# Kernel tuning notes

Hardware: AMD Instinct MI355X
Metric: run time of the kernel (lower is better)

Reference implementation:

```python
import jax, jax.numpy as jnp
import numpy as np

B, F, S, H1, H2 = 4096, 512, 32, 64, 32


def setup_inputs() -> dict:
    key = jax.random.key(0)
    ks = jax.random.split(key, 9)
    x = jax.random.normal(ks[0], (B, F), dtype=jnp.float32)
    # ExU layer init: truncated_normal(mean=4, std=0.5) on weight, std=0.5 on bias
    W0 = 4.0 + 0.5 * jax.random.normal(ks[1], (F, S, S), dtype=jnp.float32)
    b0 = 0.5 * jax.random.normal(ks[2], (F, S), dtype=jnp.float32)
    # ReLU hidden layers: xavier-ish weights, small biases
    W1 = jax.random.normal(ks[3], (F, S, H1), dtype=jnp.float32) * np.sqrt(2.0 / (S + H1))
    b1 = 0.5 * jax.random.normal(ks[4], (F, S), dtype=jnp.float32)
    W2 = jax.random.normal(ks[5], (F, H1, H2), dtype=jnp.float32) * np.sqrt(2.0 / (H1 + H2))
    b2 = 0.5 * jax.random.normal(ks[6], (F, H1), dtype=jnp.float32)
    Wl = jax.random.normal(ks[7], (F, H2), dtype=jnp.float32) * np.sqrt(2.0 / (H2 + 1))
    out_bias = jnp.zeros((1,), dtype=jnp.float32)
    return {"x": x, "W0": W0, "b0": b0, "W1": W1, "b1": b1,
            "W2": W2, "b2": b2, "Wl": Wl, "out_bias": out_bias}


def reference(x, W0, b0, W1, b1, W2, b2, Wl, out_bias):
    # ExU shallow layer per feature: clip((x_f - b0_f) @ exp(W0_f), 0, 1)
    # x[:, :, None] - b0 broadcasts scalar feature to (B, F, S)
    h = jnp.clip(jnp.einsum('bfs,fsh->bfh', x[:, :, None] - b0[None], jnp.exp(W0)), 0.0, 1.0)
    # ReLU hidden layers: relu((h - b) @ W)
    h = jax.nn.relu(jnp.einsum('bfs,fsh->bfh', h - b1[None], W1))   # (B, F, H1)
    h = jax.nn.relu(jnp.einsum('bfh,fho->bfo', h - b2[None], W2))   # (B, F, H2)
    # per-feature Linear(H2 -> 1, no bias), concatenated over features
    f_out = jnp.einsum('bfo,fo->bf', h, Wl)                          # (B, F)
    # forward_type == 'sum' (feature_dropout is identity at inference)
    return f_out.sum(axis=-1) + out_bias[0], f_out
```

## Files before the change

### kernel.cpp

```cpp
#include <hip/hip_runtime.h>

typedef __attribute__((ext_vector_type(8))) short short8;
typedef __attribute__((ext_vector_type(4))) float f32x4;
typedef unsigned int uint32;

namespace {
constexpr int F = 512, NB = 4096;
constexpr int RB = 256;
constexpr int FPB = 4;
constexpr int NFQ = F / FPB;
constexpr size_t OFF_W1F  = 0;
constexpr size_t OFF_W2F  = OFF_W1F + (size_t)F * 4 * 64 * 16;
constexpr size_t OFF_TAB  = OFF_W2F + (size_t)F * 4 * 64 * 16;
constexpr size_t OFF_PART = OFF_TAB + (size_t)F * 160 * 4;
constexpr size_t WS_NEED  = OFF_PART + (size_t)NFQ * NB * 4;
}

__device__ __forceinline__ uint32 cvtpk(float lo, float hi) {
    uint32 r;
    asm("v_cvt_pk_bf16_f32 %0, %1, %2" : "=v"(r) : "v"(lo), "v"(hi));
    return r;
}
__device__ __forceinline__ float clip01(float v) {
    return __builtin_amdgcn_fmed3f(v, 0.f, 1.f);
}

__global__ __launch_bounds__(256) void nam_prep(
    const float* __restrict__ W0, const float* __restrict__ b0,
    const float* __restrict__ W1, const float* __restrict__ b1,
    const float* __restrict__ W2, const float* __restrict__ b2,
    char* __restrict__ ws)
{
    const int f = blockIdx.x;
    const int t = threadIdx.x;
    const int lane = t & 63, w = t >> 6, g = lane >> 4, rr = lane & 15;

    __shared__ float LW[2048];
    __shared__ float red[256], red2[256];

    const float* W0f = W0 + (size_t)f * 1024;
    const float* W1f = W1 + (size_t)f * 2048;
    const float* W2f = W2 + (size_t)f * 2048;
    float* tab = (float*)(ws + OFF_TAB) + (size_t)f * 160;
    union U8 { uint32 u[4]; short8 s8; };

    *(float4*)&LW[t * 4] = *(const float4*)&W0f[t * 4];
    __syncthreads();
    {
        int j = t & 31, sc = t >> 5;
        float a = 0.f, c = 0.f;
#pragma unroll
        for (int k = 0; k < 4; ++k) {
            int s = sc * 4 + k;
            float e = expf(LW[s * 32 + j]);
            a += e; c += b0[f * 32 + s] * e;
        }
        red[sc * 32 + j] = a; red2[sc * 32 + j] = c;
    }
    __syncthreads();
    if (t < 32) {
        float a = 0.f, c = 0.f;
#pragma unroll
        for (int k = 0; k < 8; ++k) { a += red[k * 32 + t]; c += red2[k * 32 + t]; }
        tab[t] = a; tab[32 + t] = -c;
    }
    __syncthreads();

    *(float4*)&LW[t * 4]        = *(const float4*)&W1f[t * 4];
    *(float4*)&LW[1024 + t * 4] = *(const float4*)&W1f[1024 + t * 4];
    __syncthreads();
    {
        int j = t & 63, sc = t >> 6;
        float d = 0.f;
#pragma unroll
        for (int k = 0; k < 8; ++k) {
            int s = sc * 8 + k;
            d += b1[f * 32 + s] * LW[s * 64 + j];
        }
        red[sc * 64 + j] = d;
    }
    {
        int mi = w;
        int col = 32 * (mi & 1) + 8 * (rr >> 2) + 4 * (mi >> 1) + (rr & 3);
        int base = (8 * g) * 64 + col;
        U8 v;
        v.u[0] = cvtpk(LW[base],       LW[base + 64]);
        v.u[1] = cvtpk(LW[base + 128], LW[base + 192]);
        v.u[2] = cvtpk(LW[base + 256], LW[base + 320]);
        v.u[3] = cvtpk(LW[base + 384], LW[base + 448]);
        ((short8*)(ws + OFF_W1F))[((size_t)f * 4 + mi) * 64 + lane] = v.s8;
    }
    __syncthreads();
    if (t < 64) {
        float d = red[t] + red[64 + t] + red[128 + t] + red[192 + t];
        int dst = 32 * ((t >> 2) & 1) + 16 * (t >> 5) + 4 * ((t >> 3) & 3) + (t & 3);
        tab[64 + dst] = -d;
    }
    __syncthreads();

    *(float4*)&LW[t * 4]        = *(const float4*)&W2f[t * 4];
    *(float4*)&LW[1024 + t * 4] = *(const float4*)&W2f[1024 + t * 4];
    __syncthreads();
    {
        int o = t & 31, hc = t >> 5;
        float d = 0.f;
#pragma unroll
        for (int k = 0; k < 8; ++k) {
            int h = hc * 8 + k;
            d += b2[f * 64 + h] * LW[h * 32 + o];
        }
        red[hc * 32 + o] = d;
    }
    {
        int m2 = w >> 1, kc = w & 1;
        int base = (32 * kc + 8 * g) * 32 + 16 * m2 + rr;
        U8 v;
        v.u[0] = cvtpk(LW[base],       LW[base + 32]);
        v.u[1] = cvtpk(LW[base + 64],  LW[base + 96]);
        v.u[2] = cvtpk(LW[base + 128], LW[base + 160]);
        v.u[3] = cvtpk(LW[base + 192], LW[base + 224]);
        ((short8*)(ws + OFF_W2F))[((size_t)f * 4 + m2 * 2 + kc) * 64 + lane] = v.s8;
    }
    __syncthreads();
    if (t < 32) {
        float d = 0.f;
#pragma unroll
        for (int k = 0; k < 8; ++k) d += red[k * 32 + t];
        tab[128 + t] = -d;
    }
}

__device__ __forceinline__ short8 make_hb(float xv, const f32x4& A0, const f32x4& A1,
                                          const f32x4& C0, const f32x4& C1) {
    union { uint32 u[4]; short8 s8; } hb;
    hb.u[0] = cvtpk(clip01(fmaf(xv, A0[0], C0[0])), clip01(fmaf(xv, A0[1], C0[1])));
    hb.u[1] = cvtpk(clip01(fmaf(xv, A0[2], C0[2])), clip01(fmaf(xv, A0[3], C0[3])));
    hb.u[2] = cvtpk(clip01(fmaf(xv, A1[0], C1[0])), clip01(fmaf(xv, A1[1], C1[1])));
    hb.u[3] = cvtpk(clip01(fmaf(xv, A1[2], C1[2])), clip01(fmaf(xv, A1[3], C1[3])));
    return hb.s8;
}
__device__ __forceinline__ short8 packrelu(const f32x4& x, const f32x4& y) {
    union { uint32 u[4]; short8 s8; } r;
    r.u[0] = cvtpk(fmaxf(x[0], 0.f), fmaxf(x[1], 0.f));
    r.u[1] = cvtpk(fmaxf(x[2], 0.f), fmaxf(x[3], 0.f));
    r.u[2] = cvtpk(fmaxf(y[0], 0.f), fmaxf(y[1], 0.f));
    r.u[3] = cvtpk(fmaxf(y[2], 0.f), fmaxf(y[3], 0.f));
    return r.s8;
}

__global__ __launch_bounds__(256, 4) void nam_main(
    const float* __restrict__ x, const float* __restrict__ Wl,
    const char* __restrict__ ws, float* __restrict__ fout, float* __restrict__ part)
{
    const int fq = blockIdx.y;
    const int f0 = fq * FPB;
    const int rbase = blockIdx.x * RB;
    const int t = threadIdx.x;
    const int w = t >> 6, lane = t & 63;
    const int g = lane >> 4, rr = lane & 15;
    const int f = f0 + w;

    __shared__ float sx[FPB * RB];
    __shared__ float psum[FPB * RB * 4];

    {
        float4 v = *(const float4*)(x + (size_t)(rbase + t) * F + f0);
        sx[0 * RB + t] = v.x; sx[1 * RB + t] = v.y;
        sx[2 * RB + t] = v.z; sx[3 * RB + t] = v.w;
    }

    const short8* w1img = (const short8*)(ws + OFF_W1F);
    const short8* w2img = (const short8*)(ws + OFF_W2F);
    short8 w1f[4], w2f[2][2];
#pragma unroll
    for (int mi = 0; mi < 4; ++mi) w1f[mi] = w1img[((size_t)f * 4 + mi) * 64 + lane];
#pragma unroll
    for (int m2 = 0; m2 < 2; ++m2)
#pragma unroll
        for (int kc = 0; kc < 2; ++kc)
            w2f[m2][kc] = w2img[((size_t)f * 4 + m2 * 2 + kc) * 64 + lane];

    const f32x4* tabv = (const f32x4*)((const float*)(ws + OFF_TAB) + (size_t)f * 160);
    f32x4 A0 = tabv[2 * g], A1 = tabv[2 * g + 1];
    f32x4 C0 = tabv[8 + 2 * g], C1 = tabv[8 + 2 * g + 1];
    f32x4 nd1[4];
#pragma unroll
    for (int mi = 0; mi < 4; ++mi) nd1[mi] = tabv[16 + 4 * mi + g];
    f32x4 nd2[2];
#pragma unroll
    for (int m2 = 0; m2 < 2; ++m2) nd2[m2] = tabv[32 + 4 * m2 + g];
    f32x4 wl0 = *(const f32x4*)(Wl + f * 32 + 4 * g);
    f32x4 wl1 = *(const f32x4*)(Wl + f * 32 + 16 + 4 * g);

    __syncthreads();

    const float* sxf = sx + w * RB;
    float* psw = psum + w * (RB * 4);

    for (int k = 0; k < 16; ++k) {
        float xv = sxf[16 * k + rr];
        short8 hb = make_hb(xv, A0, A1, C0, C1);

        f32x4 a0 = __builtin_amdgcn_mfma_f32_16x16x32_bf16(w1f[0], hb, nd1[0], 0, 0, 0);
        f32x4 a1 = __builtin_amdgcn_mfma_f32_16x16x32_bf16(w1f[1], hb, nd1[1], 0, 0, 0);
        f32x4 a2 = __builtin_amdgcn_mfma_f32_16x16x32_bf16(w1f[2], hb, nd1[2], 0, 0, 0);
        f32x4 a3 = __builtin_amdgcn_mfma_f32_16x16x32_bf16(w1f[3], hb, nd1[3], 0, 0, 0);

        short8 r0 = packrelu(a0, a2);
        short8 r1 = packrelu(a1, a3);

        f32x4 c0 = __builtin_amdgcn_mfma_f32_16x16x32_bf16(w2f[0][0], r0, nd2[0], 0, 0, 0);
        c0 = __builtin_amdgcn_mfma_f32_16x16x32_bf16(w2f[0][1], r1, c0, 0, 0, 0);
        f32x4 c1 = __builtin_amdgcn_mfma_f32_16x16x32_bf16(w2f[1][0], r0, nd2[1], 0, 0, 0);
        c1 = __builtin_amdgcn_mfma_f32_16x16x32_bf16(w2f[1][1], r1, c1, 0, 0, 0);

        float p = 0.f;
#pragma unroll
        for (int r = 0; r < 4; ++r) {
            p = fmaf(fmaxf(c0[r], 0.f), wl0[r], p);
            p = fmaf(fmaxf(c1[r], 0.f), wl1[r], p);
        }
        psw[(16 * k + rr) * 4 + g] = p;
    }

#pragma unroll
    for (int i = 0; i < 4; ++i) {
        int row = i * 64 + lane;
        f32x4 v = *(const f32x4*)&psw[row * 4];
        ((float*)sx)[w * RB + row] = (v[0] + v[1]) + (v[2] + v[3]);
    }

    __syncthreads();

    {
        int r = t;
        float v0 = sx[0 * RB + r], v1 = sx[1 * RB + r];
        float v2 = sx[2 * RB + r], v3 = sx[3 * RB + r];
        *(float4*)(fout + (size_t)(rbase + r) * F + f0) = make_float4(v0, v1, v2, v3);
        part[(size_t)fq * NB + rbase + r] = (v0 + v1) + (v2 + v3);
    }
}

__global__ __launch_bounds__(256) void nam_sum(const float* __restrict__ part,
                                               const float* __restrict__ ob,
                                               float* __restrict__ out0) {
    int r = blockIdx.x * 256 + threadIdx.x;
    float s = ob[0];
#pragma unroll 8
    for (int q = 0; q < NFQ; ++q) s += part[(size_t)q * NB + r];
    out0[r] = s;
}

namespace fbk { constexpr int S = 32, H1 = 64, H2 = 32, BLK = 256, ROWS = 2, P1 = 36; }
__global__ __launch_bounds__(256, 2) void fb_main(
    const float* __restrict__ x,  const float* __restrict__ W0,
    const float* __restrict__ b0, const float* __restrict__ W1,
    const float* __restrict__ b1, const float* __restrict__ W2,
    const float* __restrict__ b2, const float* __restrict__ Wl,
    float* __restrict__ fout) {
    using namespace fbk;
    const int f = blockIdx.y;
    const int bbase = blockIdx.x * (BLK * ROWS);
    const int t = threadIdx.x;
    __shared__ float W0e[S * S];
    __shared__ float W1t[H1 * P1];
    __shared__ float W2l[H1 * H2];
    __shared__ float sb0[S], sb1[S], sb2[H1];
    __shared__ float sA[S], sC[S], sd1[H1], sd2[H2], sWl[H2];
    {
        float4 wv = *reinterpret_cast<const float4*>(W0 + (size_t)f * S * S + t * 4);
        W0e[t * 4 + 0] = expf(wv.x); W0e[t * 4 + 1] = expf(wv.y);
        W0e[t * 4 + 2] = expf(wv.z); W0e[t * 4 + 3] = expf(wv.w);
    }
    if (t < S) sb0[t] = b0[f * S + t];
    else if (t < 2 * S) sb1[t - S] = b1[f * S + (t - S)];
    else if (t < 2 * S + H1) sb2[t - 2 * S] = b2[f * H1 + (t - 2 * S)];
    else if (t < 2 * S + H1 + H2) sWl[t - 2 * S - H1] = Wl[f * H2 + (t - 2 * S - H1)];
#pragma unroll
    for (int k = 0; k < (S * H1) / BLK; ++k) {
        int i = t + BLK * k; int s = i >> 6, j = i & 63;
        W1t[j * P1 + s] = W1[(size_t)f * S * H1 + i];
    }
#pragma unroll
    for (int k = 0; k < (H1 * H2) / BLK; ++k) {
        int i = t + BLK * k; W2l[i] = W2[(size_t)f * H1 * H2 + i];
    }
    __syncthreads();
    if (t < S) {
        int j = t; float a = 0.f, c = 0.f;
#pragma unroll
        for (int s = 0; s < S; ++s) { float e = W0e[s * S + j]; a += e; c += sb0[s] * e; }
        sA[j] = a; sC[j] = c;
    } else if (t >= 64 && t < 64 + H1) {
        int j = t - 64; float d = 0.f;
#pragma unroll
        for (int s = 0; s < S; ++s) d += sb1[s] * W1t[j * P1 + s];
        sd1[j] = d;
    } else if (t >= 128 && t < 128 + H2) {
        int o = t - 128; float d = 0.f;
#pragma unroll
        for (int h = 0; h < H1; ++h) d += sb2[h] * W2l[h * H2 + o];
        sd2[o] = d;
    }
    __syncthreads();
    const int ra = bbase + t, rb = bbase + BLK + t;
    const float xa = x[(size_t)ra * F + f], xb = x[(size_t)rb * F + f];
    float h0a[S], h0b[S];
#pragma unroll
    for (int j = 0; j < S; ++j) {
        float A = sA[j], C = sC[j];
        h0a[j] = fminf(fmaxf(fmaf(xa, A, -C), 0.f), 1.f);
        h0b[j] = fminf(fmaxf(fmaf(xb, A, -C), 0.f), 1.f);
    }
    float acc2a[H2], acc2b[H2];
#pragma unroll
    for (int o = 0; o < H2; ++o) { float d = sd2[o]; acc2a[o] = -d; acc2b[o] = -d; }
#pragma unroll 2
    for (int j = 0; j < H1; ++j) {
        float wr[S];
#pragma unroll
        for (int q = 0; q < S / 4; ++q)
            *reinterpret_cast<float4*>(&wr[4 * q]) = reinterpret_cast<const float4*>(&W1t[j * P1])[q];
        float d1j = sd1[j];
        float pa0 = -d1j, pa1 = 0.f, pb0 = -d1j, pb1 = 0.f;
#pragma unroll
        for (int s = 0; s < S; s += 2) {
            pa0 = fmaf(h0a[s], wr[s], pa0); pb0 = fmaf(h0b[s], wr[s], pb0);
            pa1 = fmaf(h0a[s + 1], wr[s + 1], pa1); pb1 = fmaf(h0b[s + 1], wr[s + 1], pb1);
        }
        float h1a = fmaxf(pa0 + pa1, 0.f), h1b = fmaxf(pb0 + pb1, 0.f);
        float w2r[H2];
#pragma unroll
        for (int q = 0; q < H2 / 4; ++q)
            *reinterpret_cast<float4*>(&w2r[4 * q]) = reinterpret_cast<const float4*>(&W2l[j * H2])[q];
#pragma unroll
        for (int o = 0; o < H2; ++o) {
            acc2a[o] = fmaf(h1a, w2r[o], acc2a[o]); acc2b[o] = fmaf(h1b, w2r[o], acc2b[o]);
        }
    }
    float outa = 0.f, outb = 0.f;
#pragma unroll
    for (int o = 0; o < H2; ++o) {
        outa = fmaf(fmaxf(acc2a[o], 0.f), sWl[o], outa);
        outb = fmaf(fmaxf(acc2b[o], 0.f), sWl[o], outb);
    }
    fout[(size_t)ra * F + f] = outa;
    fout[(size_t)rb * F + f] = outb;
}
__global__ __launch_bounds__(256) void fb_rowsum(
    const float* __restrict__ fout, const float* __restrict__ out_bias,
    float* __restrict__ out0) {
    const int wave = threadIdx.x >> 6, lane = threadIdx.x & 63;
    const int b = blockIdx.x * 4 + wave;
    float s = 0.f;
#pragma unroll
    for (int k = 0; k < F / 64; ++k) s += fout[(size_t)b * F + k * 64 + lane];
#pragma unroll
    for (int off = 32; off; off >>= 1) s += __shfl_down(s, off, 64);
    if (lane == 0) out0[b] = s + out_bias[0];
}

extern "C" void kernel_launch(void* const* d_in, const int* in_sizes, int n_in,
                              void* d_out, int out_size, void* d_ws, size_t ws_size,
                              hipStream_t stream) {
    const float* x  = (const float*)d_in[0];
    const float* W0 = (const float*)d_in[1];
    const float* b0 = (const float*)d_in[2];
    const float* W1 = (const float*)d_in[3];
    const float* b1 = (const float*)d_in[4];
    const float* W2 = (const float*)d_in[5];
    const float* b2 = (const float*)d_in[6];
    const float* Wl = (const float*)d_in[7];
    const float* ob = (const float*)d_in[8];

    float* out0 = (float*)d_out;
    float* fout = out0 + NB;

    if (ws_size >= WS_NEED) {
        char* ws = (char*)d_ws;
        float* part = (float*)(ws + OFF_PART);
        nam_prep<<<F, 256, 0, stream>>>(W0, b0, W1, b1, W2, b2, ws);
        nam_main<<<dim3(NB / RB, NFQ), 256, 0, stream>>>(x, Wl, ws, fout, part);
        nam_sum <<<NB / 256, 256, 0, stream>>>(part, ob, out0);
    } else {
        dim3 grid(NB / (fbk::BLK * fbk::ROWS), F);
        fb_main<<<grid, fbk::BLK, 0, stream>>>(x, W0, b0, W1, b1, W2, b2, Wl, fout);
        fb_rowsum<<<NB / 4, 256, 0, stream>>>(fout, ob, out0);
    }
}
```

Baseline: 44.95 us.

## Fuse weight-prep kernel into main kernel, computing per-feature tables per block

Removes the separate prep kernel that built bf16 MFMA weight fragments and bias/exp tables in workspace. Each main-kernel wave now computes its own feature's exp(W0) sums, folded bias terms and bf16 fragments directly from the fp32 weights, keeping the tables in shared memory. This drops one launch and the workspace round trip. In exchange the prep work is repeated across the 16 row blocks per feature, and each wave does strided scalar global loads and serial reduction loops before its main compute.

```diff
diff --git a/kernel.cpp b/kernel.cpp
--- a/kernel.cpp
+++ b/kernel.cpp
@@ -9,10 +9,7 @@
 constexpr int RB = 256;
 constexpr int FPB = 4;
 constexpr int NFQ = F / FPB;
-constexpr size_t OFF_W1F  = 0;
-constexpr size_t OFF_W2F  = OFF_W1F + (size_t)F * 4 * 64 * 16;
-constexpr size_t OFF_TAB  = OFF_W2F + (size_t)F * 4 * 64 * 16;
-constexpr size_t OFF_PART = OFF_TAB + (size_t)F * 160 * 4;
+constexpr size_t OFF_PART = 0;
 constexpr size_t WS_NEED  = OFF_PART + (size_t)NFQ * NB * 4;
 }
 
@@ -23,111 +20,6 @@
 }
 __device__ __forceinline__ float clip01(float v) {
     return __builtin_amdgcn_fmed3f(v, 0.f, 1.f);
-}
-
-__global__ __launch_bounds__(256) void nam_prep(
-    const float* __restrict__ W0, const float* __restrict__ b0,
-    const float* __restrict__ W1, const float* __restrict__ b1,
-    const float* __restrict__ W2, const float* __restrict__ b2,
-    char* __restrict__ ws)
-{
-    const int f = blockIdx.x;
-    const int t = threadIdx.x;
-    const int lane = t & 63, w = t >> 6, g = lane >> 4, rr = lane & 15;
-
-    __shared__ float LW[2048];
-    __shared__ float red[256], red2[256];
-
-    const float* W0f = W0 + (size_t)f * 1024;
-    const float* W1f = W1 + (size_t)f * 2048;
-    const float* W2f = W2 + (size_t)f * 2048;
-    float* tab = (float*)(ws + OFF_TAB) + (size_t)f * 160;
-    union U8 { uint32 u[4]; short8 s8; };
-
-    *(float4*)&LW[t * 4] = *(const float4*)&W0f[t * 4];
-    __syncthreads();
-    {
-        int j = t & 31, sc = t >> 5;
-        float a = 0.f, c = 0.f;
-#pragma unroll
-        for (int k = 0; k < 4; ++k) {
-            int s = sc * 4 + k;
-            float e = expf(LW[s * 32 + j]);
-            a += e; c += b0[f * 32 + s] * e;
-        }
-        red[sc * 32 + j] = a; red2[sc * 32 + j] = c;
-    }
-    __syncthreads();
-    if (t < 32) {
-        float a = 0.f, c = 0.f;
-#pragma unroll
-        for (int k = 0; k < 8; ++k) { a += red[k * 32 + t]; c += red2[k * 32 + t]; }
-        tab[t] = a; tab[32 + t] = -c;
-    }
-    __syncthreads();
-
-    *(float4*)&LW[t * 4]        = *(const float4*)&W1f[t * 4];
-    *(float4*)&LW[1024 + t * 4] = *(const float4*)&W1f[1024 + t * 4];
-    __syncthreads();
-    {
-        int j = t & 63, sc = t >> 6;
-        float d = 0.f;
-#pragma unroll
-        for (int k = 0; k < 8; ++k) {
-            int s = sc * 8 + k;
-            d += b1[f * 32 + s] * LW[s * 64 + j];
-        }
-        red[sc * 64 + j] = d;
-    }
-    {
-        int mi = w;
-        int col = 32 * (mi & 1) + 8 * (rr >> 2) + 4 * (mi >> 1) + (rr & 3);
-        int base = (8 * g) * 64 + col;
-        U8 v;
-        v.u[0] = cvtpk(LW[base],       LW[base + 64]);
-        v.u[1] = cvtpk(LW[base + 128], LW[base + 192]);
-        v.u[2] = cvtpk(LW[base + 256], LW[base + 320]);
-        v.u[3] = cvtpk(LW[base + 384], LW[base + 448]);
-        ((short8*)(ws + OFF_W1F))[((size_t)f * 4 + mi) * 64 + lane] = v.s8;
-    }
-    __syncthreads();
-    if (t < 64) {
-        float d = red[t] + red[64 + t] + red[128 + t] + red[192 + t];
-        int dst = 32 * ((t >> 2) & 1) + 16 * (t >> 5) + 4 * ((t >> 3) & 3) + (t & 3);
-        tab[64 + dst] = -d;
-    }
-    __syncthreads();
-
-    *(float4*)&LW[t * 4]        = *(const float4*)&W2f[t * 4];
-    *(float4*)&LW[1024 + t * 4] = *(const float4*)&W2f[1024 + t * 4];
-    __syncthreads();
-    {
-        int o = t & 31, hc = t >> 5;
-        float d = 0.f;
-#pragma unroll
-        for (int k = 0; k < 8; ++k) {
-            int h = hc * 8 + k;
-            d += b2[f * 64 + h] * LW[h * 32 + o];
-        }
-        red[hc * 32 + o] = d;
-    }
-    {
-        int m2 = w >> 1, kc = w & 1;
-        int base = (32 * kc + 8 * g) * 32 + 16 * m2 + rr;
-        U8 v;
-        v.u[0] = cvtpk(LW[base],       LW[base + 32]);
-        v.u[1] = cvtpk(LW[base + 64],  LW[base + 96]);
-        v.u[2] = cvtpk(LW[base + 128], LW[base + 160]);
-        v.u[3] = cvtpk(LW[base + 192], LW[base + 224]);
-        ((short8*)(ws + OFF_W2F))[((size_t)f * 4 + m2 * 2 + kc) * 64 + lane] = v.s8;
-    }
-    __syncthreads();
-    if (t < 32) {
-        float d = 0.f;
-#pragma unroll
-        for (int k = 0; k < 8; ++k) d += red[k * 32 + t];
-        tab[128 + t] = -d;
-    }
 }
 
 __device__ __forceinline__ short8 make_hb(float xv, const f32x4& A0, const f32x4& A1,
@@ -148,9 +40,13 @@
     return r.s8;
 }
 
-__global__ __launch_bounds__(256, 4) void nam_main(
-    const float* __restrict__ x, const float* __restrict__ Wl,
-    const char* __restrict__ ws, float* __restrict__ fout, float* __restrict__ part)
+__global__ __launch_bounds__(256, 4) void nam_fused(
+    const float* __restrict__ x,
+    const float* __restrict__ W0, const float* __restrict__ b0,
+    const float* __restrict__ W1, const float* __restrict__ b1,
+    const float* __restrict__ W2, const float* __restrict__ b2,
+    const float* __restrict__ Wl,
+    float* __restrict__ fout, float* __restrict__ part)
 {
     const int fq = blockIdx.y;
     const int f0 = fq * FPB;
@@ -162,6 +58,7 @@
 
     __shared__ float sx[FPB * RB];
     __shared__ float psum[FPB * RB * 4];
+    __shared__ __align__(16) float ptab[FPB][160];
 
     {
         float4 v = *(const float4*)(x + (size_t)(rbase + t) * F + f0);
@@ -169,18 +66,69 @@
         sx[2 * RB + t] = v.z; sx[3 * RB + t] = v.w;
     }
 
-    const short8* w1img = (const short8*)(ws + OFF_W1F);
-    const short8* w2img = (const short8*)(ws + OFF_W2F);
+    const float* W0f = W0 + (size_t)f * 1024;
+    const float* W1f = W1 + (size_t)f * 2048;
+    const float* W2f = W2 + (size_t)f * 2048;
+    float* tw = ptab[w];
+    {
+        int j = lane & 31, half = lane >> 5;
+        float a = 0.f, c = 0.f;
+#pragma unroll 4
+        for (int k = 0; k < 16; ++k) {
+            int s = half * 16 + k;
+            float e = expf(W0f[s * 32 + j]);
+            a += e; c += b0[f * 32 + s] * e;
+        }
+        a += __shfl_xor(a, 32, 64);
+        c += __shfl_xor(c, 32, 64);
+        if (lane < 32) { tw[j] = a; tw[32 + j] = -c; }
+    }
+    {
+        float d = 0.f;
+#pragma unroll 4
+        for (int s = 0; s < 32; ++s) d += b1[f * 32 + s] * W1f[s * 64 + lane];
+        int dst = 32 * ((lane >> 2) & 1) + 16 * (lane >> 5) + 4 * ((lane >> 3) & 3) + (lane & 3);
+        tw[64 + dst] = -d;
+    }
+    {
+        int o = lane & 31, half = lane >> 5;
+        float d = 0.f;
+#pragma unroll 4
+        for (int k = 0; k < 32; ++k) {
+            int h = half * 32 + k;
+            d += b2[f * 64 + h] * W2f[h * 32 + o];
+        }
+        d += __shfl_xor(d, 32, 64);
+        if (lane < 32) tw[128 + o] = -d;
+    }
+
+    union U8 { uint32 u[4]; short8 s8; };
     short8 w1f[4], w2f[2][2];
 #pragma unroll
-    for (int mi = 0; mi < 4; ++mi) w1f[mi] = w1img[((size_t)f * 4 + mi) * 64 + lane];
+    for (int mi = 0; mi < 4; ++mi) {
+        int col = 32 * (mi & 1) + 8 * (rr >> 2) + 4 * (mi >> 1) + (rr & 3);
+        const float* base = W1f + (size_t)(8 * g) * 64 + col;
+        U8 v;
+        v.u[0] = cvtpk(base[0],   base[64]);
+        v.u[1] = cvtpk(base[128], base[192]);
+        v.u[2] = cvtpk(base[256], base[320]);
+        v.u[3] = cvtpk(base[384], base[448]);
+        w1f[mi] = v.s8;
+    }
 #pragma unroll
     for (int m2 = 0; m2 < 2; ++m2)
 #pragma unroll
-        for (int kc = 0; kc < 2; ++kc)
-            w2f[m2][kc] = w2img[((size_t)f * 4 + m2 * 2 + kc) * 64 + lane];
-
-    const f32x4* tabv = (const f32x4*)((const float*)(ws + OFF_TAB) + (size_t)f * 160);
+        for (int kc = 0; kc < 2; ++kc) {
+            const float* base = W2f + (size_t)(32 * kc + 8 * g) * 32 + 16 * m2 + rr;
+            U8 v;
+            v.u[0] = cvtpk(base[0],   base[32]);
+            v.u[1] = cvtpk(base[64],  base[96]);
+            v.u[2] = cvtpk(base[128], base[160]);
+            v.u[3] = cvtpk(base[192], base[224]);
+            w2f[m2][kc] = v.s8;
+        }
+
+    const f32x4* tabv = (const f32x4*)tw;
     f32x4 A0 = tabv[2 * g], A1 = tabv[2 * g + 1];
     f32x4 C0 = tabv[8 + 2 * g], C1 = tabv[8 + 2 * g + 1];
     f32x4 nd1[4];
@@ -379,9 +327,9 @@
     if (ws_size >= WS_NEED) {
         char* ws = (char*)d_ws;
         float* part = (float*)(ws + OFF_PART);
-        nam_prep<<<F, 256, 0, stream>>>(W0, b0, W1, b1, W2, b2, ws);
-        nam_main<<<dim3(NB / RB, NFQ), 256, 0, stream>>>(x, Wl, ws, fout, part);
-        nam_sum <<<NB / 256, 256, 0, stream>>>(part, ob, out0);
+        nam_fused<<<dim3(NB / RB, NFQ), 256, 0, stream>>>(x, W0, b0, W1, b1, W2, b2, Wl,
+                                                          fout, part);
+        nam_sum<<<NB / 256, 256, 0, stream>>>(part, ob, out0);
     } else {
         dim3 grid(NB / (fbk::BLK * fbk::ROWS), F);
         fb_main<<<grid, fbk::BLK, 0, stream>>>(x, W0, b0, W1, b1, W2, b2, Wl, fout);
```

New measurement: 54.58 us. +21.4%, slower.
